# Optimization experiments

Hardware: AMD Instinct MI355X
Metric: run time of the kernel (lower is better)

The kernel has to match this reference:

```python
import jax, jax.numpy as jnp
import numpy as np

N_SEGMENTS = 64


def setup_inputs() -> dict:
    key = jax.random.key(0)
    k1, k2 = jax.random.split(key)
    B, T, d = 256, 2048, 12
    inp = jax.random.normal(k1, (B, T, d), dtype=jnp.float32)
    # lengths in [1, T] (must be >= 1, as in the torch code's length[i].item())
    length = jax.random.randint(k2, (B,), 1, T + 1, dtype=jnp.int32)
    return {"inp": inp, "length": length}


def _logsig_var(X, L, n_segments):
    """Depth-2 log-signature over n_segments slices of a ragged path.

    X: (T, d) padded path, L: scalar int valid length.
    Matches signatory.LogSignature(depth=2): channels = [increments (d),
    Levy areas A_ij for i<j in lexicographic (Lyndon word) order].
    """
    T, d = X.shape
    S = n_segments
    M = max(T, 2 * S)  # static upper bound on effective length after repeat

    # torch: if L < S+1, repeat each point k = S//L + 1 times consecutively
    expand = L < S + 1
    k = jnp.where(expand, S // L + 1, 1)
    Leff = jnp.where(expand, k * L, L)

    t = jnp.arange(M)
    idx = jnp.clip(jnp.where(expand, t // k, t), 0, L - 1)
    Xe = X[idx]  # (M, d) expanded/clamped path; entries >= Leff are repeats (unused)

    # cumulative G[t] = sum_{m < t} X_m (outer) dX_m, shape (M, d, d)
    dX = Xe[1:] - Xe[:-1]                                   # (M-1, d)
    outer = Xe[:-1, :, None] * dX[:, None, :]               # (M-1, d, d)
    G = jnp.concatenate(
        [jnp.zeros((1, d, d), X.dtype), jnp.cumsum(outer, axis=0)], axis=0
    )

    # t_vec = round(linspace(1, Leff, S+1)) (round-half-even matches python round)
    j = jnp.arange(S + 1, dtype=jnp.float32)
    tv = jnp.round(1.0 + j * (Leff - 1).astype(jnp.float32) / S).astype(jnp.int32)
    a = tv[:-1] - 1   # segment start indices (inclusive), (S,)
    b = tv[1:] - 1    # segment end indices (inclusive), (S,)

    Xa, Xb = Xe[a], Xe[b]                                   # (S, d)
    inc = Xb - Xa                                           # level-1 logsig
    # segment sum of (X_m - X_a) (outer) dX_m via prefix sums
    Gs = G[b] - G[a] - Xa[:, :, None] * inc[:, None, :]     # (S, d, d)
    A = 0.5 * (Gs - jnp.swapaxes(Gs, 1, 2))                 # Levy areas
    iu, ju = np.triu_indices(d, k=1)
    levy = A[:, iu, ju]                                     # (S, d(d-1)/2)
    return jnp.concatenate([inc, levy], axis=-1)            # (S, d + d(d-1)/2)


def reference(inp, length):
    # (B, n_segments, logsig_channels)
    return jax.vmap(lambda x, l: _logsig_var(x, l, N_SEGMENTS))(inp, length)
```

## Files before the change

kernel.cpp:

```cpp
#include <hip/hip_runtime.h>


#define BATCH 256
#define TLEN 2048
#define DCH 12
#define NSEG 64
#define NPAIR 66
#define NCH 78

__device__ __forceinline__ int tv_round(int j, int Lf) {
    int q = j * Lf;
    int base = 1 + (q >> 6);
    int r = q & 63;
    int up = (r > 32) || (r == 32 && (base & 1));
    return base + up;
}

__device__ __forceinline__ void load_row(const float* __restrict__ X, int r,
                                         float* __restrict__ v) {
    const float4* p = (const float4*)(X + r * DCH);
    float4 f0 = p[0], f1 = p[1], f2 = p[2];
    v[0] = f0.x; v[1] = f0.y; v[2]  = f0.z; v[3]  = f0.w;
    v[4] = f1.x; v[5] = f1.y; v[6]  = f1.z; v[7]  = f1.w;
    v[8] = f2.x; v[9] = f2.y; v[10] = f2.z; v[11] = f2.w;
}

__global__ __launch_bounds__(256) void logsig_kernel(
        const float* __restrict__ inp,
        const int* __restrict__ length,
        float* __restrict__ out) {
    __shared__ __align__(16) float lds_out[NSEG * NCH];

    const int batch = blockIdx.x;
    const int tid = threadIdx.x;
    const int L = length[batch];

    const float* __restrict__ X = inp + (size_t)batch * TLEN * DCH;

    const int lane = tid & 63;
    const int wave = tid >> 6;
    const int seg = wave * 16 + (lane >> 2);
    const int q4 = lane & 3;

    const bool expand = (L < NSEG + 1);
    const int k = expand ? (NSEG / L + 1) : 1;
    const int Leff = expand ? k * L : L;
    const int Lf = Leff - 1;

    const int a = tv_round(seg, Lf) - 1;
    const int b = tv_round(seg + 1, Lf) - 1;

    float acc[NPAIR];
#pragma unroll
    for (int p = 0; p < NPAIR; ++p) acc[p] = 0.0f;

    int t = a + q4;
    float x[DCH], y[DCH];
    if (t < b) {
        int r0, r1;
        if (expand) {
            r0 = min(t / k, L - 1);
            r1 = min((t + 1) / k, L - 1);
        } else {
            r0 = t;
            r1 = t + 1;
        }
        load_row(X, r0, x);
        load_row(X, r1, y);
    }
    while (t < b) {
        const int tn = t + 4;
        float xn[DCH], yn[DCH];
        if (tn < b) {
            int r0, r1;
            if (expand) {
                r0 = min(tn / k, L - 1);
                r1 = min((tn + 1) / k, L - 1);
            } else {
                r0 = tn;
                r1 = tn + 1;
            }
            load_row(X, r0, xn);
            load_row(X, r1, yn);
        }
        int p = 0;
#pragma unroll
        for (int i = 0; i < DCH - 1; ++i) {
#pragma unroll
            for (int jj = i + 1; jj < DCH; ++jj) {
                acc[p] = fmaf(x[i], y[jj], acc[p]);
                ++p;
            }
        }
        p = 0;
#pragma unroll
        for (int i = 0; i < DCH - 1; ++i) {
#pragma unroll
            for (int jj = i + 1; jj < DCH; ++jj) {
                acc[p] = fmaf(-x[jj], y[i], acc[p]);
                ++p;
            }
        }
#pragma unroll
        for (int c = 0; c < DCH; ++c) { x[c] = xn[c]; y[c] = yn[c]; }
        t = tn;
    }

#pragma unroll
    for (int p = 0; p < NPAIR; ++p) {
        acc[p] += __shfl_xor(acc[p], 1, 64);
        acc[p] += __shfl_xor(acc[p], 2, 64);
    }

    if (q4 == 0) {
        int ra, rb;
        if (expand) {
            ra = min(a / k, L - 1);
            rb = min(b / k, L - 1);
        } else {
            ra = a;
            rb = b;
        }
        float xa[DCH], xb[DCH];
        load_row(X, ra, xa);
        load_row(X, rb, xb);
        float* o = lds_out + seg * NCH;
#pragma unroll
        for (int i = 0; i < DCH; ++i) o[i] = xb[i] - xa[i];
        int p = 0;
#pragma unroll
        for (int i = 0; i < DCH - 1; ++i)
#pragma unroll
            for (int jj = i + 1; jj < DCH; ++jj) {
                o[DCH + p] = 0.5f * (acc[p] - (xa[i] * xb[jj] - xa[jj] * xb[i]));
                ++p;
            }
    }
    __syncthreads();

    {
        float4* od = (float4*)(out + (size_t)batch * NSEG * NCH);
        const float4* os = (const float4*)lds_out;
        for (int i = tid; i < (NSEG * NCH) / 4; i += 256) od[i] = os[i];
    }
}

extern "C" void kernel_launch(void* const* d_in, const int* in_sizes, int n_in,
                              void* d_out, int out_size, void* d_ws, size_t ws_size,
                              hipStream_t stream) {
    const float* inp = (const float*)d_in[0];
    const int* length = (const int*)d_in[1];
    float* out = (float*)d_out;
    logsig_kernel<<<BATCH, 256, 0, stream>>>(inp, length, out);
}
```

Measured before the change: 73.68 us.

## Double-buffer row loads two steps ahead and use DPP quad reductions

The accumulation loop now keeps two register buffers and issues loads two iterations ahead, so more memory latency is hidden behind the FMA work. The segment-endpoint rows are loaded up front by every lane rather than only after the reduction. The quad reduction switches from __shfl_xor to DPP quad_perm moves, which avoid LDS-based shuffles. In exchange, register pressure rises (four 12-float buffers on top of 66 accumulators), which could lower occupancy or cause spills.

```diff
diff --git a/kernel.cpp b/kernel.cpp
--- a/kernel.cpp
+++ b/kernel.cpp
@@ -25,6 +25,51 @@
     v[8] = f2.x; v[9] = f2.y; v[10] = f2.z; v[11] = f2.w;
 }
 
+__device__ __forceinline__ void load_pair(const float* __restrict__ X, int t,
+                                          bool expand, int k, int Lm1,
+                                          float (&x)[DCH], float (&y)[DCH]) {
+    int r0, r1;
+    if (expand) {
+        r0 = min(t / k, Lm1);
+        r1 = min((t + 1) / k, Lm1);
+    } else {
+        r0 = t;
+        r1 = t + 1;
+    }
+    load_row(X, r0, x);
+    load_row(X, r1, y);
+}
+
+__device__ __forceinline__ void accum_step(const float (&x)[DCH],
+                                           const float (&y)[DCH],
+                                           float (&acc)[NPAIR]) {
+    int p = 0;
+#pragma unroll
+    for (int i = 0; i < DCH - 1; ++i)
+#pragma unroll
+        for (int jj = i + 1; jj < DCH; ++jj) {
+            acc[p] = fmaf(x[i], y[jj], acc[p]);
+            ++p;
+        }
+    p = 0;
+#pragma unroll
+    for (int i = 0; i < DCH - 1; ++i)
+#pragma unroll
+        for (int jj = i + 1; jj < DCH; ++jj) {
+            acc[p] = fmaf(-x[jj], y[i], acc[p]);
+            ++p;
+        }
+}
+
+__device__ __forceinline__ float quad_reduce_add(float v) {
+    float s1 = __int_as_float(__builtin_amdgcn_update_dpp(
+        0, __float_as_int(v), 0xB1, 0xF, 0xF, true));
+    v += s1;
+    float s2 = __int_as_float(__builtin_amdgcn_update_dpp(
+        0, __float_as_int(v), 0x4E, 0xF, 0xF, true));
+    return v + s2;
+}
+
 __global__ __launch_bounds__(256) void logsig_kernel(
         const float* __restrict__ inp,
         const int* __restrict__ length,
@@ -34,6 +79,7 @@
     const int batch = blockIdx.x;
     const int tid = threadIdx.x;
     const int L = length[batch];
+    const int Lm1 = L - 1;
 
     const float* __restrict__ X = inp + (size_t)batch * TLEN * DCH;
 
@@ -54,76 +100,39 @@
 #pragma unroll
     for (int p = 0; p < NPAIR; ++p) acc[p] = 0.0f;
 
+    float xA[DCH], yA[DCH], xB[DCH], yB[DCH];
     int t = a + q4;
-    float x[DCH], y[DCH];
-    if (t < b) {
-        int r0, r1;
-        if (expand) {
-            r0 = min(t / k, L - 1);
-            r1 = min((t + 1) / k, L - 1);
-        } else {
-            r0 = t;
-            r1 = t + 1;
-        }
-        load_row(X, r0, x);
-        load_row(X, r1, y);
-    }
-    while (t < b) {
-        const int tn = t + 4;
-        float xn[DCH], yn[DCH];
-        if (tn < b) {
-            int r0, r1;
-            if (expand) {
-                r0 = min(tn / k, L - 1);
-                r1 = min((tn + 1) / k, L - 1);
-            } else {
-                r0 = tn;
-                r1 = tn + 1;
-            }
-            load_row(X, r0, xn);
-            load_row(X, r1, yn);
-        }
-        int p = 0;
-#pragma unroll
-        for (int i = 0; i < DCH - 1; ++i) {
-#pragma unroll
-            for (int jj = i + 1; jj < DCH; ++jj) {
-                acc[p] = fmaf(x[i], y[jj], acc[p]);
-                ++p;
-            }
-        }
-        p = 0;
-#pragma unroll
-        for (int i = 0; i < DCH - 1; ++i) {
-#pragma unroll
-            for (int jj = i + 1; jj < DCH; ++jj) {
-                acc[p] = fmaf(-x[jj], y[i], acc[p]);
-                ++p;
-            }
-        }
-#pragma unroll
-        for (int c = 0; c < DCH; ++c) { x[c] = xn[c]; y[c] = yn[c]; }
-        t = tn;
-    }
+    if (t < b) load_pair(X, t, expand, k, Lm1, xA, yA);
+    if (t + 4 < b) load_pair(X, t + 4, expand, k, Lm1, xB, yB);
 
-#pragma unroll
-    for (int p = 0; p < NPAIR; ++p) {
-        acc[p] += __shfl_xor(acc[p], 1, 64);
-        acc[p] += __shfl_xor(acc[p], 2, 64);
-    }
-
-    if (q4 == 0) {
+    float xa[DCH], xb[DCH];
+    {
         int ra, rb;
         if (expand) {
-            ra = min(a / k, L - 1);
-            rb = min(b / k, L - 1);
+            ra = min(a / k, Lm1);
+            rb = min(b / k, Lm1);
         } else {
             ra = a;
             rb = b;
         }
-        float xa[DCH], xb[DCH];
         load_row(X, ra, xa);
         load_row(X, rb, xb);
+    }
+
+    while (t < b) {
+        accum_step(xA, yA, acc);
+        if (t + 8 < b) load_pair(X, t + 8, expand, k, Lm1, xA, yA);
+        t += 4;
+        if (t >= b) break;
+        accum_step(xB, yB, acc);
+        if (t + 8 < b) load_pair(X, t + 8, expand, k, Lm1, xB, yB);
+        t += 4;
+    }
+
+#pragma unroll
+    for (int p = 0; p < NPAIR; ++p) acc[p] = quad_reduce_add(acc[p]);
+
+    if (q4 == 0) {
         float* o = lds_out + seg * NCH;
 #pragma unroll
         for (int i = 0; i < DCH; ++i) o[i] = xb[i] - xa[i];
```

Measured after the change: 73.20 us, median of 2. No clear change (-0.7%).
